# Kernel tuning notes

Measured on AMD Instinct MI355X. Metric: run time of the kernel, lower is better.

## Reference

```python
import jax, jax.numpy as jnp
import numpy as np

N, B, L, D = 11, 4, 2048, 1024
EPS = 1e-5


def _layernorm(x, g, b):
    # torch LayerNorm: biased variance over last dim
    mu = x.mean(-1, keepdims=True)
    var = x.var(-1, keepdims=True)
    return (x - mu) / jnp.sqrt(var + EPS) * g + b


def _block_attn_res(V, q, g, b):
    # V: [n, B, L, D] -- completed blocks + current partial
    K = _layernorm(V, g, b)
    logits = jnp.einsum('d,nbld->nbl', q, K)      # single pseudo-query dot
    w = jax.nn.softmax(logits, axis=0)             # softmax over block dim n
    return jnp.einsum('nbl,nbld->bld', w, V)       # weighted sum back to [B,L,D]


def setup_inputs() -> dict:
    key = jax.random.key(0)
    k0, k1, k2 = jax.random.split(key, 3)
    return {
        'streams': jax.random.normal(k0, (N, B, L, D), dtype=jnp.float32),
        'attn_q': jax.random.normal(k1, (N, D), dtype=jnp.float32) * 0.02,
        'attn_gamma': jnp.ones((N, D), dtype=jnp.float32),
        'attn_beta': jnp.zeros((N, D), dtype=jnp.float32),
        'mlp_q': jax.random.normal(k2, (N, D), dtype=jnp.float32) * 0.02,
        'mlp_gamma': jnp.ones((N, D), dtype=jnp.float32),
        'mlp_beta': jnp.zeros((N, D), dtype=jnp.float32),
    }


def reference(streams, attn_q, attn_gamma, attn_beta, mlp_q, mlp_gamma, mlp_beta):
    # streams: [N, B, L, D]; sequential over the small fixed stream count (N=11)
    n = streams.shape[0]
    blocks = []
    updated = []
    for i in range(n):
        partial = streams[i]
        V = jnp.stack(blocks + [partial], axis=0)              # [i+1, B, L, D]
        h = _block_attn_res(V, attn_q[i], attn_gamma[i], attn_beta[i])
        V2 = jnp.stack(blocks + [h], axis=0)
        h = _block_attn_res(V2, mlp_q[i], mlp_gamma[i], mlp_beta[i])
        blocks.append(partial)
        updated.append(h)
    return jnp.stack(updated, axis=0)                          # [N, B, L, D]
```

## Files before the change

kernel.cpp:

```cpp
#include <hip/hip_runtime.h>
#include <math.h>

#define NN 11
#define RR 8192
#define DD 1024
#define EPSV 1e-5f
#define PREP_TPB 256

#define OFF_SCAL 22528
#define OFF_WFRAG 22592

typedef __attribute__((ext_vector_type(8))) short short8;
typedef __attribute__((ext_vector_type(4))) float f32x4;

__device__ __forceinline__ float wave_reduce(float v) {
#pragma unroll
  for (int o = 32; o > 0; o >>= 1) v += __shfl_xor(v, o, 64);
  return v;
}

__device__ __forceinline__ unsigned cvtpk(float lo, float hi) {
  unsigned r;
  asm("v_cvt_pk_bf16_f32 %0, %1, %2" : "=v"(r) : "v"(lo), "v"(hi));
  return r;
}

__global__ __launch_bounds__(PREP_TPB) void prep_kernel(
    const float* __restrict__ aq, const float* __restrict__ ag, const float* __restrict__ ab,
    const float* __restrict__ mq, const float* __restrict__ mg, const float* __restrict__ mb,
    float* __restrict__ wvec, float* __restrict__ scal)
{
  const int j = blockIdx.x;
  const float *q, *g, *bt;
  if (j < NN) { q = aq + (size_t)j*DD;      g = ag + (size_t)j*DD;      bt = ab + (size_t)j*DD; }
  else        { q = mq + (size_t)(j-NN)*DD; g = mg + (size_t)(j-NN)*DD; bt = mb + (size_t)(j-NN)*DD; }
  const int t = threadIdx.x;
  float sqg = 0.f, sqb = 0.f;
  for (int d = t; d < DD; d += PREP_TPB) {
    float qq = q[d];
    float w  = qq * g[d];
    wvec[(size_t)j*DD + d] = w;
    sqg += w;
    sqb += qq * bt[d];
  }
  sqg = wave_reduce(sqg);
  sqb = wave_reduce(sqb);
  __shared__ float red[2][PREP_TPB/64];
  const int lane = t & 63, wid = t >> 6;
  if (lane == 0) { red[0][wid] = sqg; red[1][wid] = sqb; }
  __syncthreads();
  if (t == 0) {
    float a = 0.f, b2 = 0.f;
    for (int w = 0; w < PREP_TPB/64; ++w) { a += red[0][w]; b2 += red[1][w]; }
    scal[2*j]   = a;
    scal[2*j+1] = b2;
  }
}

__global__ __launch_bounds__(256) void prep2_kernel(
    const float* __restrict__ wvec, short* __restrict__ wfrag)
{
  const int kstep = blockIdx.x;
  const int t = threadIdx.x;
#pragma unroll
  for (int q = 0; q < 4; ++q) {
    const int idx  = t*4 + q;
    const int c    = idx >> 9;
    const int lane = (idx >> 3) & 63;
    const int e    = idx & 7;
    const int k    = kstep*32 + (lane >> 4)*8 + e;
    const int j    = c*16 + (lane & 15);
    float v = (j < 22) ? wvec[(size_t)j*DD + k] : (j == 22 ? 1.0f : 0.f);
    unsigned u = __float_as_uint(v);
    u = (u + 0x7FFFu + ((u >> 16) & 1u)) >> 16;
    wfrag[(size_t)kstep*1024 + idx] = (short)u;
  }
}

__global__ __launch_bounds__(256) void fused_kernel(
    const float* __restrict__ streams, const short* __restrict__ wfrag,
    const float* __restrict__ scal, float* __restrict__ out)
{
  __shared__ __align__(16) short xt[4*11*256];
  __shared__ float fl4[4*11*40];
  __shared__ float Cs[11][12];

  const int p  = blockIdx.x;
  const int t  = threadIdx.x;
  const int l  = t & 63;
  const int wv = t >> 6;
  const int lr = l & 15, g = l >> 4;

  short* wxt = xt + wv*2816;

  float4 xf[NN];
#pragma unroll
  for (int n = 0; n < NN; ++n)
    xf[n] = *(const float4*)(streams + ((size_t)(n*RR + p))*DD + wv*256 + l*4);
#pragma unroll
  for (int n = 0; n < NN; ++n) {
    const int byte = (n*512 + l*8) ^ ((n & 7) << 4);
    *(uint2*)((char*)wxt + byte) = make_uint2(cvtpk(xf[n].x, xf[n].y), cvtpk(xf[n].z, xf[n].w));
  }

  const int arow  = (lr < NN) ? lr : (NN-1);
  const int aswz  = (arow & 7) << 4;

  f32x4 acc0 = {0.f,0.f,0.f,0.f};
  f32x4 acc1 = {0.f,0.f,0.f,0.f};
  f32x4 acc2 = {0.f,0.f,0.f,0.f};
#pragma unroll
  for (int ksl = 0; ksl < 8; ++ksl) {
    const int byte = (arow*512 + ksl*64 + g*16) ^ aswz;
    short8 af = *(const short8*)((char*)wxt + byte);
    const size_t bo = (size_t)(wv*8 + ksl)*1024 + (size_t)l*8;
    short8 b0 = *(const short8*)(wfrag + bo);
    short8 b1 = *(const short8*)(wfrag + bo + 512);
    acc0 = __builtin_amdgcn_mfma_f32_16x16x32_bf16(af, b0, acc0, 0, 0, 0);
    acc1 = __builtin_amdgcn_mfma_f32_16x16x32_bf16(af, b1, acc1, 0, 0, 0);
    acc2 = __builtin_amdgcn_mfma_f32_16x16x32_bf16(af, af, acc2, 0, 0, 0);
  }
  {
    float* R0 = fl4 + wv*440;
#pragma unroll
    for (int r = 0; r < 4; ++r) {
      const int row = g*4 + r;
      if (row < NN) {
        float* R = R0 + row*40;
        R[lr] = acc0[r];
        if (lr <= 6)  R[16 + lr] = acc1[r];
        if (lr < NN)  R[24 + lr] = acc2[r];
      }
    }
  }
  __syncthreads();

  for (int s = t; s < 440; s += 256)
    fl4[s] = fl4[s] + fl4[440 + s] + fl4[880 + s] + fl4[1320 + s];
  __syncthreads();

  if (t < NN) {
    const int i = t;
    const float qgA = scal[2*i],      qbA = scal[2*i+1];
    const float qgM = scal[2*(NN+i)], qbM = scal[2*(NN+i)+1];

    float mu[NN], rs[NN];
#pragma unroll
    for (int n = 0; n < NN; ++n) {
      mu[n] = fl4[n*40 + 22] * (1.f/DD);
      float vr = fl4[n*40 + 24 + n] * (1.f/DD) - mu[n]*mu[n];
      rs[n] = rsqrtf(vr + EPSV);
    }

    float w1[NN], dM[NN];
    float mx = -3.0e38f;
#pragma unroll
    for (int n = 0; n < NN; ++n) {
      w1[n] = 0.f;
      if (n <= i) {
        float lg = (fl4[n*40 + i] - mu[n]*qgA)*rs[n] + qbA;
        w1[n] = lg;
        mx = fmaxf(mx, lg);
      }
    }
    float S = 0.f;
#pragma unroll
    for (int n = 0; n < NN; ++n) if (n <= i) { float e = __expf(w1[n]-mx); w1[n] = e; S += e; }
    const float inv = 1.f/S;
    float muh = 0.f, hd = 0.f;
#pragma unroll
    for (int n = 0; n < NN; ++n) {
      if (n <= i) {
        w1[n] *= inv;
        dM[n] = fl4[n*40 + 11 + i];
        muh += w1[n]*mu[n];
        hd  += w1[n]*dM[n];
      } else w1[n] = 0.f;
    }

    float hss = 0.f;
#pragma unroll
    for (int m = 0; m < NN; ++m) {
      const float wm = w1[m];
      float acc = 0.f;
#pragma unroll
      for (int n = 0; n < NN; ++n) acc = fmaf(w1[n], fl4[m*40 + 24 + n], acc);
      hss = fmaf(wm, acc, hss);
    }
    const float varh = hss*(1.f/DD) - muh*muh;
    const float rsh  = rsqrtf(varh + EPSV);
    const float lgh  = (hd - muh*qgM)*rsh + qbM;

    float lg2[NN], w2[NN];
    float mx2 = lgh;
#pragma unroll
    for (int n = 0; n < NN; ++n) if (n < i) {
      lg2[n] = (dM[n] - mu[n]*qgM)*rs[n] + qbM;
      mx2 = fmaxf(mx2, lg2[n]);
    }
    float eh = __expf(lgh - mx2);
    float S2 = eh;
#pragma unroll
    for (int n = 0; n < NN; ++n) if (n < i) { w2[n] = __expf(lg2[n]-mx2); S2 += w2[n]; }
    const float inv2 = 1.f/S2;
    const float ehw  = eh*inv2;
#pragma unroll
    for (int n = 0; n < NN; ++n) {
      float cc = ehw * w1[n];
      if (n < i) cc += w2[n]*inv2;
      Cs[i][n] = cc;
    }
  }
  __syncthreads();

  const int kt = wv*256 + l*4;
#pragma unroll
  for (int i = 0; i < NN; ++i) {
    float o0 = 0.f, o1 = 0.f, o2 = 0.f, o3 = 0.f;
#pragma unroll
    for (int n = 0; n < NN; ++n) {
      const float c = Cs[i][n];
      o0 = fmaf(c, xf[n].x, o0);
      o1 = fmaf(c, xf[n].y, o1);
      o2 = fmaf(c, xf[n].z, o2);
      o3 = fmaf(c, xf[n].w, o3);
    }
    *(float4*)(out + ((size_t)(i*RR + p))*DD + kt) = make_float4(o0, o1, o2, o3);
  }
}

extern "C" void kernel_launch(void* const* d_in, const int* in_sizes, int n_in,
                              void* d_out, int out_size, void* d_ws, size_t ws_size,
                              hipStream_t stream) {
  const float* streams = (const float*)d_in[0];
  const float* aq = (const float*)d_in[1];
  const float* ag = (const float*)d_in[2];
  const float* ab = (const float*)d_in[3];
  const float* mq = (const float*)d_in[4];
  const float* mg = (const float*)d_in[5];
  const float* mb = (const float*)d_in[6];
  float* outp = (float*)d_out;

  float* wsf   = (float*)d_ws;
  float* wvec  = wsf;
  float* scal  = wsf + OFF_SCAL;
  short* wfrag = (short*)(wsf + OFF_WFRAG);

  prep_kernel<<<dim3(2*NN), dim3(PREP_TPB), 0, stream>>>(aq, ag, ab, mq, mg, mb, wvec, scal);
  prep2_kernel<<<dim3(32), dim3(256), 0, stream>>>(wvec, wfrag);
  fused_kernel<<<dim3(RR), dim3(256), 0, stream>>>(streams, wfrag, scal, outp);
}
```

Measured before the change: 209.7 us.

## Double-buffer stream chunks through LDS and re-read inputs for the output pass

```diff
diff --git a/kernel.cpp b/kernel.cpp
--- a/kernel.cpp
+++ b/kernel.cpp
@@ -81,7 +81,7 @@
     const float* __restrict__ streams, const short* __restrict__ wfrag,
     const float* __restrict__ scal, float* __restrict__ out)
 {
-  __shared__ __align__(16) short xt[4*11*256];
+  __shared__ __align__(16) short xb[2][2816];
   __shared__ float fl4[4*11*40];
   __shared__ float Cs[11][12];
 
@@ -90,36 +90,55 @@
   const int l  = t & 63;
   const int wv = t >> 6;
   const int lr = l & 15, g = l >> 4;
-
-  short* wxt = xt + wv*2816;
-
-  float4 xf[NN];
-#pragma unroll
-  for (int n = 0; n < NN; ++n)
-    xf[n] = *(const float4*)(streams + ((size_t)(n*RR + p))*DD + wv*256 + l*4);
-#pragma unroll
-  for (int n = 0; n < NN; ++n) {
-    const int byte = (n*512 + l*8) ^ ((n & 7) << 4);
-    *(uint2*)((char*)wxt + byte) = make_uint2(cvtpk(xf[n].x, xf[n].y), cvtpk(xf[n].z, xf[n].w));
-  }
-
-  const int arow  = (lr < NN) ? lr : (NN-1);
-  const int aswz  = (arow & 7) << 4;
+  const int arow = (lr < NN) ? lr : (NN-1);
+  const int aswz = (arow & 7) << 4;
+
+#pragma unroll
+  for (int ii = 0; ii < 3; ++ii) {
+    const int idx = ii*256 + t;
+    if (idx < 704) {
+      const int row = idx >> 6, col = idx & 63;
+      float4 v = *(const float4*)(streams + ((size_t)row*RR + p)*DD + col*4);
+      const int byte = (row*512 + col*8) ^ ((row & 7) << 4);
+      *(uint2*)((char*)xb[0] + byte) = make_uint2(cvtpk(v.x, v.y), cvtpk(v.z, v.w));
+    }
+  }
+  __syncthreads();
 
   f32x4 acc0 = {0.f,0.f,0.f,0.f};
   f32x4 acc1 = {0.f,0.f,0.f,0.f};
   f32x4 acc2 = {0.f,0.f,0.f,0.f};
-#pragma unroll
-  for (int ksl = 0; ksl < 8; ++ksl) {
-    const int byte = (arow*512 + ksl*64 + g*16) ^ aswz;
-    short8 af = *(const short8*)((char*)wxt + byte);
-    const size_t bo = (size_t)(wv*8 + ksl)*1024 + (size_t)l*8;
-    short8 b0 = *(const short8*)(wfrag + bo);
-    short8 b1 = *(const short8*)(wfrag + bo + 512);
-    acc0 = __builtin_amdgcn_mfma_f32_16x16x32_bf16(af, b0, acc0, 0, 0, 0);
-    acc1 = __builtin_amdgcn_mfma_f32_16x16x32_bf16(af, b1, acc1, 0, 0, 0);
-    acc2 = __builtin_amdgcn_mfma_f32_16x16x32_bf16(af, af, acc2, 0, 0, 0);
-  }
+
+  for (int c = 0; c < 4; ++c) {
+    if (c < 3) {
+#pragma unroll
+      for (int ii = 0; ii < 3; ++ii) {
+        const int idx = ii*256 + t;
+        if (idx < 704) {
+          const int row = idx >> 6, col = idx & 63;
+          float4 v = *(const float4*)(streams + ((size_t)row*RR + p)*DD + (c+1)*256 + col*4);
+          const int byte = (row*512 + col*8) ^ ((row & 7) << 4);
+          *(uint2*)((char*)xb[(c+1)&1] + byte) = make_uint2(cvtpk(v.x, v.y), cvtpk(v.z, v.w));
+        }
+      }
+    }
+
+    const char* cb = (const char*)xb[c & 1];
+#pragma unroll
+    for (int j = 0; j < 2; ++j) {
+      const int ksc = 2*wv + j;
+      const int byte = (arow*512 + ksc*64 + g*16) ^ aswz;
+      short8 af = *(const short8*)(cb + byte);
+      const size_t bo = (size_t)(c*8 + ksc)*1024 + (size_t)l*8;
+      short8 b0 = *(const short8*)(wfrag + bo);
+      short8 b1 = *(const short8*)(wfrag + bo + 512);
+      acc0 = __builtin_amdgcn_mfma_f32_16x16x32_bf16(af, b0, acc0, 0, 0, 0);
+      acc1 = __builtin_amdgcn_mfma_f32_16x16x32_bf16(af, b1, acc1, 0, 0, 0);
+      acc2 = __builtin_amdgcn_mfma_f32_16x16x32_bf16(af, af, acc2, 0, 0, 0);
+    }
+    __syncthreads();
+  }
+
   {
     float* R0 = fl4 + wv*440;
 #pragma unroll
@@ -213,20 +232,24 @@
   }
   __syncthreads();
 
-  const int kt = wv*256 + l*4;
-#pragma unroll
-  for (int i = 0; i < NN; ++i) {
-    float o0 = 0.f, o1 = 0.f, o2 = 0.f, o3 = 0.f;
-#pragma unroll
-    for (int n = 0; n < NN; ++n) {
-      const float c = Cs[i][n];
-      o0 = fmaf(c, xf[n].x, o0);
-      o1 = fmaf(c, xf[n].y, o1);
-      o2 = fmaf(c, xf[n].z, o2);
-      o3 = fmaf(c, xf[n].w, o3);
-    }
-    *(float4*)(out + ((size_t)(i*RR + p))*DD + kt) = make_float4(o0, o1, o2, o3);
-  }
+  float4 o[NN];
+#pragma unroll
+  for (int i = 0; i < NN; ++i) o[i] = make_float4(0.f, 0.f, 0.f, 0.f);
+#pragma unroll
+  for (int n = 0; n < NN; ++n) {
+    float4 x = *(const float4*)(streams + ((size_t)n*RR + p)*DD + t*4);
+#pragma unroll
+    for (int i = 0; i < NN; ++i) {
+      const float cc = Cs[i][n];
+      o[i].x = fmaf(cc, x.x, o[i].x);
+      o[i].y = fmaf(cc, x.y, o[i].y);
+      o[i].z = fmaf(cc, x.z, o[i].z);
+      o[i].w = fmaf(cc, x.w, o[i].w);
+    }
+  }
+#pragma unroll
+  for (int i = 0; i < NN; ++i)
+    *(float4*)(out + ((size_t)(i*RR + p))*DD + t*4) = o[i];
 }
 
 extern "C" void kernel_launch(void* const* d_in, const int* in_sizes, int n_in,
```

Result: slower. 262.3 us (+25.1%).

## Assign one row per wave to remove block-level syncs and cross-wave reduction

Applied to the files above, without the earlier changes.

```diff
diff --git a/kernel.cpp b/kernel.cpp
--- a/kernel.cpp
+++ b/kernel.cpp
@@ -81,74 +81,66 @@
     const float* __restrict__ streams, const short* __restrict__ wfrag,
     const float* __restrict__ scal, float* __restrict__ out)
 {
-  __shared__ __align__(16) short xt[4*11*256];
-  __shared__ float fl4[4*11*40];
-  __shared__ float Cs[11][12];
-
-  const int p  = blockIdx.x;
+  __shared__ __align__(16) short xt[4*2816];
+  __shared__ float flw[4*396];
+  __shared__ float Csw[4*132];
+
   const int t  = threadIdx.x;
   const int l  = t & 63;
   const int wv = t >> 6;
+  const int p  = blockIdx.x*4 + wv;
   const int lr = l & 15, g = l >> 4;
-
-  short* wxt = xt + wv*2816;
-
-  float4 xf[NN];
-#pragma unroll
-  for (int n = 0; n < NN; ++n)
-    xf[n] = *(const float4*)(streams + ((size_t)(n*RR + p))*DD + wv*256 + l*4);
-#pragma unroll
-  for (int n = 0; n < NN; ++n) {
-    const int byte = (n*512 + l*8) ^ ((n & 7) << 4);
-    *(uint2*)((char*)wxt + byte) = make_uint2(cvtpk(xf[n].x, xf[n].y), cvtpk(xf[n].z, xf[n].w));
-  }
-
-  const int arow  = (lr < NN) ? lr : (NN-1);
-  const int aswz  = (arow & 7) << 4;
+  const int arow = (lr < NN) ? lr : (NN-1);
+  const int aswz = (arow & 7) << 4;
+
+  short* wxb = xt  + wv*2816;
+  float* R   = flw + wv*396;
+  float* Cw  = Csw + wv*132;
 
   f32x4 acc0 = {0.f,0.f,0.f,0.f};
   f32x4 acc1 = {0.f,0.f,0.f,0.f};
   f32x4 acc2 = {0.f,0.f,0.f,0.f};
-#pragma unroll
-  for (int ksl = 0; ksl < 8; ++ksl) {
-    const int byte = (arow*512 + ksl*64 + g*16) ^ aswz;
-    short8 af = *(const short8*)((char*)wxt + byte);
-    const size_t bo = (size_t)(wv*8 + ksl)*1024 + (size_t)l*8;
-    short8 b0 = *(const short8*)(wfrag + bo);
-    short8 b1 = *(const short8*)(wfrag + bo + 512);
-    acc0 = __builtin_amdgcn_mfma_f32_16x16x32_bf16(af, b0, acc0, 0, 0, 0);
-    acc1 = __builtin_amdgcn_mfma_f32_16x16x32_bf16(af, b1, acc1, 0, 0, 0);
-    acc2 = __builtin_amdgcn_mfma_f32_16x16x32_bf16(af, af, acc2, 0, 0, 0);
-  }
-  {
-    float* R0 = fl4 + wv*440;
-#pragma unroll
-    for (int r = 0; r < 4; ++r) {
-      const int row = g*4 + r;
-      if (row < NN) {
-        float* R = R0 + row*40;
-        R[lr] = acc0[r];
-        if (lr <= 6)  R[16 + lr] = acc1[r];
-        if (lr < NN)  R[24 + lr] = acc2[r];
-      }
-    }
-  }
-  __syncthreads();
-
-  for (int s = t; s < 440; s += 256)
-    fl4[s] = fl4[s] + fl4[440 + s] + fl4[880 + s] + fl4[1320 + s];
-  __syncthreads();
-
-  if (t < NN) {
-    const int i = t;
+
+  for (int c = 0; c < 4; ++c) {
+#pragma unroll
+    for (int n = 0; n < NN; ++n) {
+      float4 v = *(const float4*)(streams + ((size_t)n*RR + p)*DD + c*256 + l*4);
+      const int byte = (n*512 + l*8) ^ ((n & 7) << 4);
+      *(uint2*)((char*)wxb + byte) = make_uint2(cvtpk(v.x, v.y), cvtpk(v.z, v.w));
+    }
+#pragma unroll
+    for (int ks = 0; ks < 8; ++ks) {
+      const int byte = (arow*512 + ks*64 + g*16) ^ aswz;
+      short8 af = *(const short8*)((char*)wxb + byte);
+      const size_t bo = (size_t)(c*8 + ks)*1024 + (size_t)l*8;
+      short8 b0 = *(const short8*)(wfrag + bo);
+      short8 b1 = *(const short8*)(wfrag + bo + 512);
+      acc0 = __builtin_amdgcn_mfma_f32_16x16x32_bf16(af, b0, acc0, 0, 0, 0);
+      acc1 = __builtin_amdgcn_mfma_f32_16x16x32_bf16(af, b1, acc1, 0, 0, 0);
+      acc2 = __builtin_amdgcn_mfma_f32_16x16x32_bf16(af, af, acc2, 0, 0, 0);
+    }
+  }
+
+#pragma unroll
+  for (int r = 0; r < 4; ++r) {
+    const int row = g*4 + r;
+    if (row < NN) {
+      R[row*36 + lr] = acc0[r];
+      if (lr <= 6) R[row*36 + 16 + lr] = acc1[r];
+      if (lr < NN) R[row*36 + 24 + lr] = acc2[r];
+    }
+  }
+
+  if (l < NN) {
+    const int i = l;
     const float qgA = scal[2*i],      qbA = scal[2*i+1];
     const float qgM = scal[2*(NN+i)], qbM = scal[2*(NN+i)+1];
 
     float mu[NN], rs[NN];
 #pragma unroll
     for (int n = 0; n < NN; ++n) {
-      mu[n] = fl4[n*40 + 22] * (1.f/DD);
-      float vr = fl4[n*40 + 24 + n] * (1.f/DD) - mu[n]*mu[n];
+      mu[n] = R[n*36 + 22] * (1.f/DD);
+      float vr = R[n*36 + 24 + n] * (1.f/DD) - mu[n]*mu[n];
       rs[n] = rsqrtf(vr + EPSV);
     }
 
@@ -158,7 +150,7 @@
     for (int n = 0; n < NN; ++n) {
       w1[n] = 0.f;
       if (n <= i) {
-        float lg = (fl4[n*40 + i] - mu[n]*qgA)*rs[n] + qbA;
+        float lg = (R[n*36 + i] - mu[n]*qgA)*rs[n] + qbA;
         w1[n] = lg;
         mx = fmaxf(mx, lg);
       }
@@ -172,7 +164,7 @@
     for (int n = 0; n < NN; ++n) {
       if (n <= i) {
         w1[n] *= inv;
-        dM[n] = fl4[n*40 + 11 + i];
+        dM[n] = R[n*36 + 11 + i];
         muh += w1[n]*mu[n];
         hd  += w1[n]*dM[n];
       } else w1[n] = 0.f;
@@ -184,7 +176,7 @@
       const float wm = w1[m];
       float acc = 0.f;
 #pragma unroll
-      for (int n = 0; n < NN; ++n) acc = fmaf(w1[n], fl4[m*40 + 24 + n], acc);
+      for (int n = 0; n < NN; ++n) acc = fmaf(w1[n], R[m*36 + 24 + n], acc);
       hss = fmaf(wm, acc, hss);
     }
     const float varh = hss*(1.f/DD) - muh*muh;
@@ -208,24 +200,28 @@
     for (int n = 0; n < NN; ++n) {
       float cc = ehw * w1[n];
       if (n < i) cc += w2[n]*inv2;
-      Cs[i][n] = cc;
-    }
-  }
-  __syncthreads();
-
-  const int kt = wv*256 + l*4;
-#pragma unroll
-  for (int i = 0; i < NN; ++i) {
-    float o0 = 0.f, o1 = 0.f, o2 = 0.f, o3 = 0.f;
-#pragma unroll
-    for (int n = 0; n < NN; ++n) {
-      const float c = Cs[i][n];
-      o0 = fmaf(c, xf[n].x, o0);
-      o1 = fmaf(c, xf[n].y, o1);
-      o2 = fmaf(c, xf[n].z, o2);
-      o3 = fmaf(c, xf[n].w, o3);
-    }
-    *(float4*)(out + ((size_t)(i*RR + p))*DD + kt) = make_float4(o0, o1, o2, o3);
+      Cw[i*12 + n] = cc;
+    }
+  }
+
+  for (int c = 0; c < 4; ++c) {
+    float4 x[NN];
+#pragma unroll
+    for (int n = 0; n < NN; ++n)
+      x[n] = *(const float4*)(streams + ((size_t)n*RR + p)*DD + c*256 + l*4);
+#pragma unroll
+    for (int i = 0; i < NN; ++i) {
+      float o0 = 0.f, o1 = 0.f, o2 = 0.f, o3 = 0.f;
+#pragma unroll
+      for (int n = 0; n < NN; ++n) {
+        const float cc = Cw[i*12 + n];
+        o0 = fmaf(cc, x[n].x, o0);
+        o1 = fmaf(cc, x[n].y, o1);
+        o2 = fmaf(cc, x[n].z, o2);
+        o3 = fmaf(cc, x[n].w, o3);
+      }
+      *(float4*)(out + ((size_t)(i*RR + p))*DD + c*256 + l*4) = make_float4(o0, o1, o2, o3);
+    }
   }
 }
 
@@ -248,5 +244,5 @@
 
   prep_kernel<<<dim3(2*NN), dim3(PREP_TPB), 0, stream>>>(aq, ag, ab, mq, mg, mb, wvec, scal);
   prep2_kernel<<<dim3(32), dim3(256), 0, stream>>>(wvec, wfrag);
-  fused_kernel<<<dim3(RR), dim3(256), 0, stream>>>(streams, wfrag, scal, outp);
-}
+  fused_kernel<<<dim3(RR/4), dim3(256), 0, stream>>>(streams, wfrag, scal, outp);
+}
```

Measured after the change: 319.6 us. 1.52x slower.
